# Kernel optimization log

Measured on AMD Instinct MI355X. Metric: run time of the kernel, lower is better.

The kernel has to match this reference:

```python
import jax, jax.numpy as jnp
import numpy as np
from jax import lax

POOL_SIZE = 7
MERGE_INTERVAL = 1
NUM_FRAMES = 16_777_216  # 2**24, indices exact in float32
MAX_BEATS = NUM_FRAMES // 8  # fixed upper bound on number of merged-peak sections


def setup_inputs() -> dict:
    key = jax.random.key(0)
    logit = jax.random.normal(key, (1, NUM_FRAMES), dtype=jnp.float32)
    return {"logit": logit}


def reference(logit):
    # logit: (1, N)
    x = logit[0]  # (N,)
    N = x.shape[0]
    pad = POOL_SIZE // 2
    # max_pool1d, stride 1, same padding
    pooled = lax.reduce_window(x, -jnp.inf, lax.max,
                               window_dimensions=(POOL_SIZE,),
                               window_strides=(1,),
                               padding=((pad, pad),))
    # peak: position is a local max within the window AND value > 0
    peak = (x == pooled) & (x > 0)  # (N,) bool

    idx = jnp.arange(N, dtype=jnp.int32)
    # position of the most recent peak at or before each index (-1 if none)
    last_peak = lax.cummax(jnp.where(peak, idx, jnp.int32(-1)))
    # previous peak strictly before each index
    prev_peak = jnp.concatenate([jnp.full((1,), -1, jnp.int32), last_peak[:-1]])
    gap = idx - prev_peak
    # a peak starts a new section if gap to previous peak > merge_interval (first peak always new)
    is_new = peak & ((gap > MERGE_INTERVAL) | (prev_peak < 0))
    # section id per position (valid only at peaks); sections are contiguous 0..S-1
    section = jnp.cumsum(is_new.astype(jnp.int32)) - 1
    # route non-peaks to an overflow bucket
    seg_ids = jnp.where(peak, section, jnp.int32(MAX_BEATS))

    peak_f = peak.astype(jnp.float32)
    sum_peaks = jax.ops.segment_sum(idx.astype(jnp.float32) * peak_f, seg_ids,
                                    num_segments=MAX_BEATS + 1,
                                    indices_are_sorted=True)[:MAX_BEATS]
    count_peaks = jax.ops.segment_sum(peak_f, seg_ids,
                                      num_segments=MAX_BEATS + 1,
                                      indices_are_sorted=True)[:MAX_BEATS]
    # averaged beat positions; unused sections padded with -1 (torch returns a
    # dynamically-sized (1, num_sections) tensor; here first num_sections entries match)
    beats = jnp.where(count_peaks > 0,
                      sum_peaks / jnp.maximum(count_peaks, 1.0),
                      jnp.float32(-1.0))
    return beats[None, :]  # (1, MAX_BEATS)
```

## Files before the change

### kernel.cpp

```cpp
#include <hip/hip_runtime.h>
#include <cstdint>
#include <math.h>

#define N_FRAMES 16777216
#define MAX_BEATS (N_FRAMES / 8)
#define CHUNK 4096
#define NTHREADS 256
#define NCHUNK (N_FRAMES / CHUNK)
#define NBLK (NCHUNK / 4)
#define TOTAL_MASKS ((size_t)NCHUNK * 64)

typedef unsigned long long u64;
typedef unsigned int u32;

__device__ __forceinline__ float max3f(float a, float b, float c) {
  return fmaxf(fmaxf(a, b), c);
}

__global__ __launch_bounds__(NTHREADS) void k_count(const float* __restrict__ x,
                                                    int* __restrict__ counts,
                                                    u64* __restrict__ masks) {
  __shared__ u32 m16[NTHREADS];
  __shared__ u32 s_pm1;
  const int b = blockIdx.x;
  const int g0 = b * CHUNK;
  const int t = threadIdx.x;
  const int gbase = g0 + t * 16;

  float v[24];
  if (gbase - 4 >= 0 && gbase + 20 <= N_FRAMES) {
    const float4* p = reinterpret_cast<const float4*>(x + gbase - 4);
#pragma unroll
    for (int k = 0; k < 6; ++k) {
      const float4 f = p[k];
      v[4 * k + 0] = f.x; v[4 * k + 1] = f.y; v[4 * k + 2] = f.z; v[4 * k + 3] = f.w;
    }
  } else {
#pragma unroll
    for (int k = 0; k < 24; ++k) {
      const int gi = gbase - 4 + k;
      v[k] = (gi >= 0 && gi < N_FRAMES) ? x[gi] : -INFINITY;
    }
  }

  float Lt[21];
#pragma unroll
  for (int i = 0; i < 21; ++i) Lt[i] = max3f(v[i], v[i + 1], v[i + 2]);

  u32 pm = 0;
#pragma unroll
  for (int e = 0; e < 16; ++e) {
    const float c = v[e + 4];
    const float m = fmaxf(Lt[e + 1], Lt[e + 5]);
    if (c > 0.0f && c >= m) pm |= (1u << e);
  }
  m16[t] = pm;
  if (t == 0) {
    const float c = v[3];
    const float m = fmaxf(Lt[0], Lt[4]);
    s_pm1 = (c > 0.0f && c >= m) ? 1u : 0u;
  }
  __syncthreads();

  if (t < 64) {
    const u64 m = (u64)m16[4 * t] | ((u64)m16[4 * t + 1] << 16) |
                  ((u64)m16[4 * t + 2] << 32) | ((u64)m16[4 * t + 3] << 48);
    masks[((size_t)b << 6) + t] = m;
    const u64 carry = (t == 0) ? (u64)s_pm1 : (u64)((m16[4 * t - 1] >> 15) & 1u);
    int cnt = __popcll(m & ~((m << 1) | carry));
#pragma unroll
    for (int off = 32; off; off >>= 1) cnt += __shfl_down(cnt, off, 64);
    if (t == 0) counts[b] = cnt;
  }
}

__global__ __launch_bounds__(NTHREADS) void k_emit(const u64* __restrict__ masks,
                                                   const int* __restrict__ counts,
                                                   float* __restrict__ out) {
  __shared__ int s_wtot[4];
  __shared__ int s_texcl[NTHREADS];
  __shared__ int s_off[4];
  __shared__ int s_total;
  const int t = threadIdx.x, lane = t & 63, wv = t >> 6;

  int s = 0;
  const int cb = t * 16;
#pragma unroll
  for (int e = 0; e < 16; ++e) s += counts[cb + e];
  int incl = s;
#pragma unroll
  for (int off = 1; off < 64; off <<= 1) {
    const int vv = __shfl_up(incl, off, 64);
    if (lane >= off) incl += vv;
  }
  s_texcl[t] = incl - s;
  if (lane == 63) s_wtot[wv] = incl;
  __syncthreads();
  if (t == 0) s_total = s_wtot[0] + s_wtot[1] + s_wtot[2] + s_wtot[3];
  if (t < 4) {
    const int target = blockIdx.x * 4 + t;
    const int j = target >> 4, r = target & 15;
    int wb = 0;
    for (int ww = 0; ww < (j >> 6); ++ww) wb += s_wtot[ww];
    int pfx = wb + s_texcl[j];
    for (int e = 0; e < r; ++e) pfx += counts[j * 16 + e];
    s_off[t] = pfx;
  }
  __syncthreads();

  const int b = blockIdx.x * 4 + wv;
  const size_t mi = ((size_t)b << 6) + lane;
  const u64 m = masks[mi];
  const u32 myb63 = (u32)(m >> 63);
  u32 prevb = __shfl_up(myb63, 1, 64);
  if (lane == 0) prevb = (b == 0) ? 0u : (u32)(masks[mi - 1] >> 63);
  u64 sm = m & ~((m << 1) | (u64)prevb);
  const int cnt = __popcll(sm);

  int incl2 = cnt;
#pragma unroll
  for (int off = 1; off < 64; off <<= 1) {
    const int vv = __shfl_up(incl2, off, 64);
    if (lane >= off) incl2 += vv;
  }
  int sid = s_off[wv] + incl2 - cnt;

  if (s_off[wv] < MAX_BEATS) {
    const int gbase = b * CHUNK + lane * 64;
    while (sm) {
      const int sb = __builtin_ctzll(sm);
      sm &= sm - 1;
      const int i0 = gbase + sb;
      const u64 above = m >> sb;
      const int len = (~above == 0ull) ? (64 - sb) : __builtin_ctzll(~above);
      int end = i0 + len - 1;
      if (sb + len == 64) {
        size_t idx = mi + 1;
        while (idx < TOTAL_MASKS) {
          const u64 mm = masks[idx];
          if (~mm == 0ull) { end += 64; ++idx; }
          else { end += __builtin_ctzll(~mm); break; }
        }
      }
      if (sid < MAX_BEATS)
        out[sid] = (float)(((double)i0 + (double)end) * 0.5);
      ++sid;
    }
  }

  const int lo = blockIdx.x * (MAX_BEATS / NBLK);
  const int hi = lo + (MAX_BEATS / NBLK);
  for (int i = max(lo, s_total) + t; i < hi; i += NTHREADS)
    out[i] = -1.0f;
}

extern "C" void kernel_launch(void* const* d_in, const int* in_sizes, int n_in,
                              void* d_out, int out_size, void* d_ws, size_t ws_size,
                              hipStream_t stream) {
  const float* x = (const float*)d_in[0];
  float* out = (float*)d_out;

  u64* masks = (u64*)d_ws;
  int* counts = (int*)(masks + TOTAL_MASKS);

  k_count<<<NCHUNK, NTHREADS, 0, stream>>>(x, counts, masks);
  k_emit<<<NBLK, NTHREADS, 0, stream>>>(masks, counts, out);
}
```

Measured before the change: 28.43 us.

## Process two 4K chunks per block with wave-shuffle mask packing

```diff
diff --git a/kernel.cpp b/kernel.cpp
--- a/kernel.cpp
+++ b/kernel.cpp
@@ -7,6 +7,8 @@
 #define CHUNK 4096
 #define NTHREADS 256
 #define NCHUNK (N_FRAMES / CHUNK)
+#define BCHUNK 8192
+#define NCBLK (N_FRAMES / BCHUNK)
 #define NBLK (NCHUNK / 4)
 #define TOTAL_MASKS ((size_t)NCHUNK * 64)
 
@@ -17,16 +19,8 @@
   return fmaxf(fmaxf(a, b), c);
 }
 
-__global__ __launch_bounds__(NTHREADS) void k_count(const float* __restrict__ x,
-                                                    int* __restrict__ counts,
-                                                    u64* __restrict__ masks) {
-  __shared__ u32 m16[NTHREADS];
-  __shared__ u32 s_pm1;
-  const int b = blockIdx.x;
-  const int g0 = b * CHUNK;
-  const int t = threadIdx.x;
-  const int gbase = g0 + t * 16;
-
+__device__ __forceinline__ void stencil16(const float* __restrict__ x, int gbase,
+                                          u32& pm, u32& pm1) {
   float v[24];
   if (gbase - 4 >= 0 && gbase + 20 <= N_FRAMES) {
     const float4* p = reinterpret_cast<const float4*>(x + gbase - 4);
@@ -42,35 +36,57 @@
       v[k] = (gi >= 0 && gi < N_FRAMES) ? x[gi] : -INFINITY;
     }
   }
-
   float Lt[21];
 #pragma unroll
   for (int i = 0; i < 21; ++i) Lt[i] = max3f(v[i], v[i + 1], v[i + 2]);
-
-  u32 pm = 0;
+  pm = 0;
 #pragma unroll
   for (int e = 0; e < 16; ++e) {
     const float c = v[e + 4];
     const float m = fmaxf(Lt[e + 1], Lt[e + 5]);
     if (c > 0.0f && c >= m) pm |= (1u << e);
   }
-  m16[t] = pm;
+  const float cm1 = v[3];
+  pm1 = (cm1 > 0.0f && cm1 >= fmaxf(Lt[0], Lt[4])) ? 1u : 0u;
+}
+
+__device__ __forceinline__ int do_segment(const float* __restrict__ x,
+                                          u64* __restrict__ masks,
+                                          int chunk4k, int wv, int lane, int gbase) {
+  u32 pm, pm1;
+  stencil16(x, gbase, pm, pm1);
+  const int cnt = __popc(pm & ~((pm << 1) | pm1));
+  const u32 a = __shfl(pm, 4 * lane + 0, 64);
+  const u32 b = __shfl(pm, 4 * lane + 1, 64);
+  const u32 c = __shfl(pm, 4 * lane + 2, 64);
+  const u32 d = __shfl(pm, 4 * lane + 3, 64);
+  if (lane < 16) {
+    const u64 m = (u64)a | ((u64)b << 16) | ((u64)c << 32) | ((u64)d << 48);
+    masks[((size_t)chunk4k << 6) + 16 * wv + lane] = m;
+  }
+  return cnt;
+}
+
+__global__ __launch_bounds__(NTHREADS) void k_count(const float* __restrict__ x,
+                                                    int* __restrict__ counts,
+                                                    u64* __restrict__ masks) {
+  __shared__ u32 s_pack[4];
+  const int b = blockIdx.x;
+  const int t = threadIdx.x, lane = t & 63, wv = t >> 6;
+  const int B = b * BCHUNK;
+
+  const int cntA = do_segment(x, masks, 2 * b,     wv, lane, B + 1024 * wv + 16 * lane);
+  const int cntB = do_segment(x, masks, 2 * b + 1, wv, lane, B + 4096 + 1024 * wv + 16 * lane);
+
+  u32 packed = (u32)cntA | ((u32)cntB << 16);
+#pragma unroll
+  for (int off = 32; off; off >>= 1) packed += __shfl_down(packed, off, 64);
+  if (lane == 0) s_pack[wv] = packed;
+  __syncthreads();
   if (t == 0) {
-    const float c = v[3];
-    const float m = fmaxf(Lt[0], Lt[4]);
-    s_pm1 = (c > 0.0f && c >= m) ? 1u : 0u;
-  }
-  __syncthreads();
-
-  if (t < 64) {
-    const u64 m = (u64)m16[4 * t] | ((u64)m16[4 * t + 1] << 16) |
-                  ((u64)m16[4 * t + 2] << 32) | ((u64)m16[4 * t + 3] << 48);
-    masks[((size_t)b << 6) + t] = m;
-    const u64 carry = (t == 0) ? (u64)s_pm1 : (u64)((m16[4 * t - 1] >> 15) & 1u);
-    int cnt = __popcll(m & ~((m << 1) | carry));
-#pragma unroll
-    for (int off = 32; off; off >>= 1) cnt += __shfl_down(cnt, off, 64);
-    if (t == 0) counts[b] = cnt;
+    const u32 p = s_pack[0] + s_pack[1] + s_pack[2] + s_pack[3];
+    counts[2 * b]     = (int)(p & 0xFFFFu);
+    counts[2 * b + 1] = (int)(p >> 16);
   }
 }
 
@@ -163,6 +179,6 @@
   u64* masks = (u64*)d_ws;
   int* counts = (int*)(masks + TOTAL_MASKS);
 
-  k_count<<<NCHUNK, NTHREADS, 0, stream>>>(x, counts, masks);
+  k_count<<<NCBLK, NTHREADS, 0, stream>>>(x, counts, masks);
   k_emit<<<NBLK, NTHREADS, 0, stream>>>(masks, counts, out);
 }
```

Measured after the change: 28.94 us. About the same (+1.8%).

## Share halo values via wave shuffles and stage emitted beats in LDS

Applied to the files above, without the earlier changes.

```diff
diff --git a/kernel.cpp b/kernel.cpp
--- a/kernel.cpp
+++ b/kernel.cpp
@@ -9,6 +9,7 @@
 #define NCHUNK (N_FRAMES / CHUNK)
 #define NBLK (NCHUNK / 4)
 #define TOTAL_MASKS ((size_t)NCHUNK * 64)
+#define MAXSEC 2064
 
 typedef unsigned long long u64;
 typedef unsigned int u32;
@@ -23,24 +24,37 @@
   __shared__ u32 m16[NTHREADS];
   __shared__ u32 s_pm1;
   const int b = blockIdx.x;
-  const int g0 = b * CHUNK;
   const int t = threadIdx.x;
-  const int gbase = g0 + t * 16;
+  const int lane = t & 63;
+  const int gbase = b * CHUNK + t * 16;
 
-  float v[24];
-  if (gbase - 4 >= 0 && gbase + 20 <= N_FRAMES) {
-    const float4* p = reinterpret_cast<const float4*>(x + gbase - 4);
+  float v[23];
+  {
+    const float4* p = reinterpret_cast<const float4*>(x + gbase);
 #pragma unroll
-    for (int k = 0; k < 6; ++k) {
+    for (int k = 0; k < 4; ++k) {
       const float4 f = p[k];
-      v[4 * k + 0] = f.x; v[4 * k + 1] = f.y; v[4 * k + 2] = f.z; v[4 * k + 3] = f.w;
+      v[4 + 4 * k] = f.x; v[5 + 4 * k] = f.y; v[6 + 4 * k] = f.z; v[7 + 4 * k] = f.w;
     }
-  } else {
-#pragma unroll
-    for (int k = 0; k < 24; ++k) {
-      const int gi = gbase - 4 + k;
-      v[k] = (gi >= 0 && gi < N_FRAMES) ? x[gi] : -INFINITY;
-    }
+  }
+  v[0]  = __shfl_up(v[16], 1, 64);
+  v[1]  = __shfl_up(v[17], 1, 64);
+  v[2]  = __shfl_up(v[18], 1, 64);
+  v[3]  = __shfl_up(v[19], 1, 64);
+  v[20] = __shfl_down(v[4], 1, 64);
+  v[21] = __shfl_down(v[5], 1, 64);
+  v[22] = __shfl_down(v[6], 1, 64);
+  if (lane == 0) {
+    if (gbase >= 4) {
+      const float4 f = *reinterpret_cast<const float4*>(x + gbase - 4);
+      v[0] = f.x; v[1] = f.y; v[2] = f.z; v[3] = f.w;
+    } else { v[0] = v[1] = v[2] = v[3] = -INFINITY; }
+  }
+  if (lane == 63) {
+    if (gbase + 20 <= N_FRAMES) {
+      const float4 f = *reinterpret_cast<const float4*>(x + gbase + 16);
+      v[20] = f.x; v[21] = f.y; v[22] = f.z;
+    } else { v[20] = v[21] = v[22] = -INFINITY; }
   }
 
   float Lt[21];
@@ -77,6 +91,7 @@
 __global__ __launch_bounds__(NTHREADS) void k_emit(const u64* __restrict__ masks,
                                                    const int* __restrict__ counts,
                                                    float* __restrict__ out) {
+  __shared__ float s_out[4][MAXSEC];
   __shared__ int s_wtot[4];
   __shared__ int s_texcl[NTHREADS];
   __shared__ int s_off[4];
@@ -123,13 +138,15 @@
     const int vv = __shfl_up(incl2, off, 64);
     if (lane >= off) incl2 += vv;
   }
-  int sid = s_off[wv] + incl2 - cnt;
+  const int cnt_chunk = __shfl(incl2, 63, 64);
+  int sidl = incl2 - cnt;
 
   if (s_off[wv] < MAX_BEATS) {
     const int gbase = b * CHUNK + lane * 64;
-    while (sm) {
-      const int sb = __builtin_ctzll(sm);
-      sm &= sm - 1;
+    u64 smw = sm;
+    while (smw) {
+      const int sb = __builtin_ctzll(smw);
+      smw &= smw - 1;
       const int i0 = gbase + sb;
       const u64 above = m >> sb;
       const int len = (~above == 0ull) ? (64 - sb) : __builtin_ctzll(~above);
@@ -142,9 +159,17 @@
           else { end += __builtin_ctzll(~mm); break; }
         }
       }
-      if (sid < MAX_BEATS)
-        out[sid] = (float)(((double)i0 + (double)end) * 0.5);
-      ++sid;
+      s_out[wv][sidl] = (float)(((double)i0 + (double)end) * 0.5);
+      ++sidl;
+    }
+  }
+  __syncthreads();
+
+  if (s_off[wv] < MAX_BEATS) {
+    const int off0 = s_off[wv];
+    for (int i = lane; i < cnt_chunk; i += 64) {
+      const int gi = off0 + i;
+      if (gi < MAX_BEATS) out[gi] = s_out[wv][i];
     }
   }
 
```

Measured after the change: 26.72 us. 6.0% less time.
